# Kernel tuning notes

Measured on AMD Instinct MI355X. Metric: run time of the kernel, lower is better.

Reference implementation:

```python
import jax, jax.numpy as jnp
import numpy as np

NEG_SLOPE = 0.2
EPS = 1e-8
N, E, IN_F, OUT_F, H = 50000, 800000, 256, 32, 8


def setup_inputs() -> dict:
    key = jax.random.key(0)
    k1, k2, k3, k4, k5 = jax.random.split(key, 5)
    x = jax.random.normal(k1, (N, IN_F), dtype=jnp.float32)
    edge_index = jax.random.randint(k2, (2, E), 0, N, dtype=jnp.int32)
    # xavier_uniform bounds as in torch reset_parameters
    bw = float(np.sqrt(6.0 / (IN_F + OUT_F)))
    W = jax.random.uniform(k3, (H, IN_F, OUT_F), minval=-bw, maxval=bw, dtype=jnp.float32)
    ba = float(np.sqrt(6.0 / (OUT_F + 1)))
    a_src = jax.random.uniform(k4, (H, OUT_F), minval=-ba, maxval=ba, dtype=jnp.float32)
    a_dst = jax.random.uniform(k5, (H, OUT_F), minval=-ba, maxval=ba, dtype=jnp.float32)
    return {"x": x, "edge_index": edge_index, "W": W, "a_src": a_src, "a_dst": a_dst}


def reference(x, edge_index, W, a_src, a_dst):
    num_nodes = x.shape[0]
    src, dst = edge_index[0], edge_index[1]
    # per-head linear transform: [H, N, F]
    h = jnp.einsum('ni,hif->hnf', x, W)
    # per-node attention logits (a_src/a_dst are the squeezed [H,F] vectors)
    s_src = jnp.einsum('hnf,hf->hn', h, a_src)  # [H, N]
    s_dst = jnp.einsum('hnf,hf->hn', h, a_dst)  # [H, N]
    # edge scores + LeakyReLU, laid out [E, H] for segment ops
    ea = (s_src[:, src] + s_dst[:, dst]).T  # [E, H]
    ea = jnp.where(ea > 0, ea, NEG_SLOPE * ea)
    # sparse softmax over incoming edges of each destination node
    m = jax.ops.segment_max(ea, dst, num_segments=num_nodes)  # [N, H]
    ea = jnp.exp(ea - m[dst])
    s = jax.ops.segment_sum(ea, dst, num_segments=num_nodes)  # [N, H]
    ea = ea / (s[dst] + EPS)  # [E, H]
    # weighted scatter-add aggregation (dropout is identity in eval)
    hn = jnp.transpose(h, (1, 0, 2))  # [N, H, F]
    wf = hn[src] * ea[:, :, None]  # [E, H, F]
    out = jax.ops.segment_sum(wf, dst, num_segments=num_nodes)  # [N, H, F]
    # concat heads -> [N, H*F]
    return out.reshape(num_nodes, -1)
```

## Files before the change

### kernel.cpp

```cpp
#include <hip/hip_runtime.h>
#include <stdint.h>

#define NN 50000
#define EE 800000
#define INF_ 256
#define OUTF 32
#define HH 8
#define NEG_SLOPE 0.2f
#define EPS_ 1e-8f
#define CAP 48

typedef unsigned short u16;
typedef unsigned int u32;
typedef short bf16x8 __attribute__((ext_vector_type(8)));
typedef float f32x4 __attribute__((ext_vector_type(4)));

__device__ __forceinline__ float bflo(u32 w){ return __uint_as_float(w << 16); }
__device__ __forceinline__ float bfhi(u32 w){ return __uint_as_float(w & 0xFFFF0000u); }
__device__ __forceinline__ u16 f2bf(float f){
  u32 u = __float_as_uint(f);
  u += 0x7FFFu + ((u >> 16) & 1u);
  return (u16)(u >> 16);
}

__global__ void k_prep(const float* __restrict__ W, const float* __restrict__ a_src,
                       const float* __restrict__ a_dst, u16* __restrict__ Wt){
  int n = blockIdx.x;
  int t = threadIdx.x;
  int k4 = t * 4;
  ushort4 o;
  if (n < 256){
    int h = n >> 5, f = n & 31;
    const float* Wh = W + h*(INF_*OUTF) + f;
    o.x = f2bf(Wh[(k4+0)*OUTF]);
    o.y = f2bf(Wh[(k4+1)*OUTF]);
    o.z = f2bf(Wh[(k4+2)*OUTF]);
    o.w = f2bf(Wh[(k4+3)*OUTF]);
  } else {
    int j = n - 256;
    int h = j >> 1;
    const float* av = (j & 1) ? (a_dst + h*OUTF) : (a_src + h*OUTF);
    const float* Wh = W + h*(INF_*OUTF);
    float r[4];
#pragma unroll
    for (int i=0;i<4;i++){
      const float4* Wk = (const float4*)(Wh + (k4+i)*OUTF);
      const float4* A4 = (const float4*)av;
      float s = 0.f;
#pragma unroll
      for (int q=0;q<8;q++){
        float4 w = Wk[q], a = A4[q];
        s += w.x*a.x + w.y*a.y + w.z*a.z + w.w*a.w;
      }
      r[i] = s;
    }
    o.x=f2bf(r[0]); o.y=f2bf(r[1]); o.z=f2bf(r[2]); o.w=f2bf(r[3]);
  }
  *(ushort4*)(Wt + n*INF_ + k4) = o;
}

#define BM 64
#define BK 32
#define NB 272
#define LDA 56

__global__ __launch_bounds__(256, 2) void k_gemm(const float* __restrict__ x,
    const u16* __restrict__ Wt, u16* __restrict__ h_out,
    float* __restrict__ s_src, float* __restrict__ s_dst){
  __shared__ __align__(16) u16 As[BM*LDA];
  __shared__ __align__(16) u16 Bs[NB*LDA];
  int tid = threadIdx.x;
  int n0 = blockIdx.x * BM;
  int wv = tid >> 6, lane = tid & 63;
  int lr = lane & 15, lg = lane >> 4;

  f32x4 zero4 = {0.f,0.f,0.f,0.f};
  f32x4 acc[4][4];
  f32x4 acc2[4];
#pragma unroll
  for (int m=0;m<4;m++){
    acc2[m] = zero4;
#pragma unroll
    for (int n=0;n<4;n++) acc[m][n] = zero4;
  }

  int a_row = tid >> 3;
  int a_c4  = tid & 7;
  u32 a_off = (u32)a_row*LDA + (a_c4&3)*8 + (a_c4>>2)*4;

  float4 a_reg[2];
  uint4  b_reg[5];

#pragma unroll
  for (int i=0;i<2;i++){
    int n = n0 + a_row + i*32;
    a_reg[i] = (n < NN) ? *(const float4*)(x + n*INF_ + a_c4*4)
                        : make_float4(0.f,0.f,0.f,0.f);
  }
#pragma unroll
  for (int i=0;i<5;i++){
    int idx = tid + i*256;
    if (idx < NB*4){
      int col = idx >> 2, c16 = idx & 3;
      b_reg[i] = *(const uint4*)(Wt + col*INF_ + c16*8);
    }
  }

  for (int step = 0; step < 8; ++step){
    __syncthreads();
#pragma unroll
    for (int i=0;i<2;i++){
      float4 u = a_reg[i];
      ushort4 o; o.x=f2bf(u.x); o.y=f2bf(u.y); o.z=f2bf(u.z); o.w=f2bf(u.w);
      *(ushort4*)(As + a_off + i*32*LDA) = o;
    }
#pragma unroll
    for (int i=0;i<5;i++){
      int idx = tid + i*256;
      if (idx < NB*4){
        int col = idx >> 2, c16 = idx & 3;
        u32 off = (u32)col*LDA + (c16&1)*16 + (c16>>1)*4;
        uint4 b = b_reg[i];
        *(uint2*)(Bs + off)     = make_uint2(b.x, b.y);
        *(uint2*)(Bs + off + 8) = make_uint2(b.z, b.w);
      }
    }
    __syncthreads();
    if (step < 7){
      int k0 = (step+1)*BK;
#pragma unroll
      for (int i=0;i<2;i++){
        int n = n0 + a_row + i*32;
        a_reg[i] = (n < NN) ? *(const float4*)(x + n*INF_ + k0 + a_c4*4)
                            : make_float4(0.f,0.f,0.f,0.f);
      }
#pragma unroll
      for (int i=0;i<5;i++){
        int idx = tid + i*256;
        if (idx < NB*4){
          int col = idx >> 2, c16 = idx & 3;
          b_reg[i] = *(const uint4*)(Wt + col*INF_ + k0 + c16*8);
        }
      }
    }
    bf16x8 af[4];
#pragma unroll
    for (int m=0;m<4;m++)
      af[m] = *(const bf16x8*)(As + (m*16+lr)*LDA + lg*8);
    int cb = wv*64;
#pragma unroll
    for (int n=0;n<4;n++){
      bf16x8 bv = *(const bf16x8*)(Bs + (cb + n*16 + lr)*LDA + lg*8);
#pragma unroll
      for (int m=0;m<4;m++)
        acc[m][n] = __builtin_amdgcn_mfma_f32_16x16x32_bf16(af[m], bv, acc[m][n], 0, 0, 0);
    }
    if (wv == 0){
      bf16x8 b2 = *(const bf16x8*)(Bs + (256 + lr)*LDA + lg*8);
#pragma unroll
      for (int m=0;m<4;m++)
        acc2[m] = __builtin_amdgcn_mfma_f32_16x16x32_bf16(af[m], b2, acc2[m], 0, 0, 0);
    }
  }

#pragma unroll
  for (int m=0;m<4;m++){
#pragma unroll
    for (int r=0;r<4;r++){
      int row = m*16 + lg*4 + r;
      int n = n0 + row;
      if (n >= NN) continue;
      u16* dst = h_out + n*INF_ + wv*64 + lr;
      dst[0]  = f2bf(acc[m][0][r]);
      dst[16] = f2bf(acc[m][1][r]);
      dst[32] = f2bf(acc[m][2][r]);
      dst[48] = f2bf(acc[m][3][r]);
    }
  }
  if (wv == 0){
    int h = lr >> 1;
    float* sp = (lr & 1) ? s_dst : s_src;
#pragma unroll
    for (int m=0;m<4;m++){
#pragma unroll
      for (int r=0;r<4;r++){
        int n = n0 + m*16 + lg*4 + r;
        if (n < NN) sp[n*8 + h] = acc2[m][r];
      }
    }
  }
}

__global__ void k_append(const int* __restrict__ ei, int* __restrict__ cnt,
                         int* __restrict__ slots){
  int e = blockIdx.x*blockDim.x + threadIdx.x;
  if (e < EE){
    int d = ei[EE + e];
    int pos = atomicAdd(&cnt[d], 1);
    if (pos < CAP) slots[d*CAP + pos] = ei[e];
  }
}

__global__ __launch_bounds__(256) void k_agg(const int* __restrict__ cnt,
    const int* __restrict__ slots, const float* __restrict__ s_src,
    const float* __restrict__ s_dst, const u16* __restrict__ h_bf,
    float* __restrict__ out){
  int lane = threadIdx.x & 63;
  int n = blockIdx.x*4 + (threadIdx.x >> 6);
  if (n >= NN) return;
  int h = lane >> 3, q = lane & 7;
  int d = cnt[n]; if (d > CAP) d = CAP;
  float sd = s_dst[n*8 + h];
  int my_src = (lane < d) ? slots[n*CAP + lane] : 0;
  const u16* hb = h_bf + h*32 + q*4;
  float l = 0.f;
  float a0=0.f, a1=0.f, a2=0.f, a3=0.f;
  for (int e0 = 0; e0 < d; e0 += 8){
    int se[8];
#pragma unroll
    for (int i=0;i<8;i++) se[i] = __shfl(my_src, e0 + i, 64);
    float vs[8];
#pragma unroll
    for (int i=0;i<8;i++) vs[i] = s_src[se[i]*8 + h];
    uint2 v[8];
#pragma unroll
    for (int i=0;i<8;i++) v[i] = *(const uint2*)(hb + se[i]*INF_);
#pragma unroll
    for (int i=0;i<8;i++){
      float sc = vs[i] + sd;
      sc = fmaxf(sc, NEG_SLOPE*sc);
      float p = (e0 + i < d) ? __expf(sc) : 0.f;
      l += p;
      a0 += p*bflo(v[i].x);
      a1 += p*bfhi(v[i].x);
      a2 += p*bflo(v[i].y);
      a3 += p*bfhi(v[i].y);
    }
  }
  float inv = 1.f/(l + EPS_);
  float4 o = make_float4(a0*inv, a1*inv, a2*inv, a3*inv);
  *(float4*)(out + n*INF_ + h*32 + q*4) = o;
}

extern "C" void kernel_launch(void* const* d_in, const int* in_sizes, int n_in,
                              void* d_out, int out_size, void* d_ws, size_t ws_size,
                              hipStream_t stream){
  const float* x     = (const float*)d_in[0];
  const int*   ei    = (const int*)d_in[1];
  const float* W     = (const float*)d_in[2];
  const float* a_src = (const float*)d_in[3];
  const float* a_dst = (const float*)d_in[4];
  float* out = (float*)d_out;
  char* ws = (char*)d_ws;

  u16*   h_bf    = (u16*)  (ws + 0);
  float* s_src   = (float*)(ws + 25600000);
  float* s_dst   = (float*)(ws + 27200000);
  int*   cnt     = (int*)  (ws + 28800000);
  int*   slots   = (int*)  (ws + 29000064);
  u16*   Wt      = (u16*)  (ws + 29000064);

  (void)hipMemsetAsync(cnt, 0, NN*sizeof(int), stream);
  k_prep<<<NB, 64, 0, stream>>>(W, a_src, a_dst, Wt);
  k_gemm<<<(NN + BM - 1)/BM, 256, 0, stream>>>(x, Wt, h_bf, s_src, s_dst);
  k_append<<<EE/256, 256, 0, stream>>>(ei, cnt, slots);
  k_agg<<<(NN + 3)/4, 256, 0, stream>>>(cnt, slots, s_src, s_dst, h_bf, out);
}
```

Measured before the change: 239.7 us.

## Fuse edge bucketing into GEMM launch, compact slots, widen aggregation loads

The memset of the degree counters moves into the weight-prep kernel, whose block size grows from 64 to 256 threads to cover all nodes. Edge bucketing (atomic append per destination) now runs as extra blocks of the GEMM launch, so both proceed concurrently in one kernel. Neighbor slots are stored as 16-bit indices, which relies on the node count staying below 65536. The aggregation kernel splits each node's edges between the two half-waves, loads 16 bytes of features per lane per edge, and combines the two halves with a cross-lane shuffle. Together these cut launch count, memset overhead, slot traffic and gather instruction count.

```diff
diff --git a/kernel.cpp b/kernel.cpp
--- a/kernel.cpp
+++ b/kernel.cpp
@@ -24,9 +24,13 @@
 }
 
 __global__ void k_prep(const float* __restrict__ W, const float* __restrict__ a_src,
-                       const float* __restrict__ a_dst, u16* __restrict__ Wt){
+                       const float* __restrict__ a_dst, u16* __restrict__ Wt,
+                       int* __restrict__ cnt){
   int n = blockIdx.x;
   int t = threadIdx.x;
+  int z = n*256 + t;
+  if (z < NN) cnt[z] = 0;
+  if (t >= 64) return;
   int k4 = t * 4;
   ushort4 o;
   if (n < 256){
@@ -63,13 +67,27 @@
 #define BK 32
 #define NB 272
 #define LDA 56
-
-__global__ __launch_bounds__(256, 2) void k_gemm(const float* __restrict__ x,
+#define GEMM_B 782
+#define APP_B  3125
+
+__global__ __launch_bounds__(256, 2) void k_ga(const float* __restrict__ x,
     const u16* __restrict__ Wt, u16* __restrict__ h_out,
-    float* __restrict__ s_src, float* __restrict__ s_dst){
+    float* __restrict__ s_src, float* __restrict__ s_dst,
+    const int* __restrict__ ei, int* __restrict__ cnt, u16* __restrict__ slots){
   __shared__ __align__(16) u16 As[BM*LDA];
   __shared__ __align__(16) u16 Bs[NB*LDA];
   int tid = threadIdx.x;
+
+  if (blockIdx.x >= GEMM_B){
+    int e = (blockIdx.x - GEMM_B)*256 + tid;
+    if (e < EE){
+      int d = ei[EE + e];
+      int pos = atomicAdd(&cnt[d], 1);
+      if (pos < CAP) slots[d*CAP + pos] = (u16)ei[e];
+    }
+    return;
+  }
+
   int n0 = blockIdx.x * BM;
   int wv = tid >> 6, lane = tid & 63;
   int lr = lane & 15, lg = lane >> 4;
@@ -191,55 +209,51 @@
   }
 }
 
-__global__ void k_append(const int* __restrict__ ei, int* __restrict__ cnt,
-                         int* __restrict__ slots){
-  int e = blockIdx.x*blockDim.x + threadIdx.x;
-  if (e < EE){
-    int d = ei[EE + e];
-    int pos = atomicAdd(&cnt[d], 1);
-    if (pos < CAP) slots[d*CAP + pos] = ei[e];
-  }
-}
-
 __global__ __launch_bounds__(256) void k_agg(const int* __restrict__ cnt,
-    const int* __restrict__ slots, const float* __restrict__ s_src,
+    const u16* __restrict__ slots, const float* __restrict__ s_src,
     const float* __restrict__ s_dst, const u16* __restrict__ h_bf,
     float* __restrict__ out){
   int lane = threadIdx.x & 63;
   int n = blockIdx.x*4 + (threadIdx.x >> 6);
   if (n >= NN) return;
-  int h = lane >> 3, q = lane & 7;
+  int eh = lane >> 5;
+  int hh = (lane >> 2) & 7;
+  int q4 = lane & 3;
   int d = cnt[n]; if (d > CAP) d = CAP;
-  float sd = s_dst[n*8 + h];
-  int my_src = (lane < d) ? slots[n*CAP + lane] : 0;
-  const u16* hb = h_bf + h*32 + q*4;
+  float sd = s_dst[n*8 + hh];
+  int my_src = (lane < d) ? (int)slots[n*CAP + lane] : 0;
+  const u16* hb = h_bf + hh*32 + q4*8;
   float l = 0.f;
-  float a0=0.f, a1=0.f, a2=0.f, a3=0.f;
+  float a[8];
+#pragma unroll
+  for (int k=0;k<8;k++) a[k] = 0.f;
   for (int e0 = 0; e0 < d; e0 += 8){
-    int se[8];
-#pragma unroll
-    for (int i=0;i<8;i++) se[i] = __shfl(my_src, e0 + i, 64);
-    float vs[8];
-#pragma unroll
-    for (int i=0;i<8;i++) vs[i] = s_src[se[i]*8 + h];
-    uint2 v[8];
-#pragma unroll
-    for (int i=0;i<8;i++) v[i] = *(const uint2*)(hb + se[i]*INF_);
-#pragma unroll
-    for (int i=0;i<8;i++){
+    int se[4]; float vs[4]; uint4 v[4];
+#pragma unroll
+    for (int i=0;i<4;i++) se[i] = __shfl(my_src, e0 + 2*i + eh, 64);
+#pragma unroll
+    for (int i=0;i<4;i++) v[i] = *(const uint4*)(hb + se[i]*INF_);
+#pragma unroll
+    for (int i=0;i<4;i++) vs[i] = s_src[se[i]*8 + hh];
+#pragma unroll
+    for (int i=0;i<4;i++){
       float sc = vs[i] + sd;
       sc = fmaxf(sc, NEG_SLOPE*sc);
-      float p = (e0 + i < d) ? __expf(sc) : 0.f;
+      float p = (e0 + 2*i + eh < d) ? __expf(sc) : 0.f;
       l += p;
-      a0 += p*bflo(v[i].x);
-      a1 += p*bfhi(v[i].x);
-      a2 += p*bflo(v[i].y);
-      a3 += p*bfhi(v[i].y);
-    }
-  }
+      a[0] += p*bflo(v[i].x); a[1] += p*bfhi(v[i].x);
+      a[2] += p*bflo(v[i].y); a[3] += p*bfhi(v[i].y);
+      a[4] += p*bflo(v[i].z); a[5] += p*bfhi(v[i].z);
+      a[6] += p*bflo(v[i].w); a[7] += p*bfhi(v[i].w);
+    }
+  }
+  l += __shfl_xor(l, 32, 64);
+#pragma unroll
+  for (int k=0;k<8;k++) a[k] += __shfl_xor(a[k], 32, 64);
   float inv = 1.f/(l + EPS_);
-  float4 o = make_float4(a0*inv, a1*inv, a2*inv, a3*inv);
-  *(float4*)(out + n*INF_ + h*32 + q*4) = o;
+  float4 o = make_float4(a[eh*4+0]*inv, a[eh*4+1]*inv,
+                         a[eh*4+2]*inv, a[eh*4+3]*inv);
+  *(float4*)(out + n*INF_ + hh*32 + q4*8 + eh*4) = o;
 }
 
 extern "C" void kernel_launch(void* const* d_in, const int* in_sizes, int n_in,
@@ -257,12 +271,10 @@
   float* s_src   = (float*)(ws + 25600000);
   float* s_dst   = (float*)(ws + 27200000);
   int*   cnt     = (int*)  (ws + 28800000);
-  int*   slots   = (int*)  (ws + 29000064);
-  u16*   Wt      = (u16*)  (ws + 29000064);
-
-  (void)hipMemsetAsync(cnt, 0, NN*sizeof(int), stream);
-  k_prep<<<NB, 64, 0, stream>>>(W, a_src, a_dst, Wt);
-  k_gemm<<<(NN + BM - 1)/BM, 256, 0, stream>>>(x, Wt, h_bf, s_src, s_dst);
-  k_append<<<EE/256, 256, 0, stream>>>(ei, cnt, slots);
+  u16*   slots   = (u16*)  (ws + 29000064);
+  u16*   Wt      = (u16*)  (ws + 33800064);
+
+  k_prep<<<NB, 256, 0, stream>>>(W, a_src, a_dst, Wt, cnt);
+  k_ga<<<GEMM_B + APP_B, 256, 0, stream>>>(x, Wt, h_bf, s_src, s_dst, ei, cnt, slots);
   k_agg<<<(NN + 3)/4, 256, 0, stream>>>(cnt, slots, s_src, s_dst, h_bf, out);
 }
```

Result: faster. 232.6 us (-3.0%).
